# Optimization experiments

Measured on AMD Instinct MI355X. Metric: run time of the kernel, lower is better.

Reference implementation:

```python
import jax, jax.numpy as jnp
import numpy as np
from jax import lax

NBINS = 10
PP = 8            # pixels_per_cell
CPB = 2           # cells_per_block
MAX_ANGLE = float(np.pi)
EPS = 1e-5


def setup_inputs() -> dict:
    key = jax.random.key(0)
    img = jax.random.uniform(key, (32, 1, 512, 512), dtype=jnp.float32)
    # fixed Sobel-like gradient filters, same as the torch buffer: (2,1,3,3) OIHW
    m = np.array([[1.0, 0.0, -1.0], [2.0, 0.0, -2.0], [1.0, 0.0, -1.0]], dtype=np.float32)
    weight = jnp.asarray(np.stack([m, m.T])[:, None, :, :])
    return {"img": img, "weight": weight}


def reference(img, weight):
    n, _, H, W = img.shape
    # gradient conv: padding=1, stride=1 keeps spatial size
    gxy = lax.conv_general_dilated(
        img, weight, window_strides=(1, 1), padding=[(1, 1), (1, 1)],
        dimension_numbers=("NCHW", "OIHW", "NCHW"))  # (n,2,H,W)
    mag = jnp.sqrt(jnp.sum(gxy * gxy, axis=1))          # (n,H,W)
    phase = jnp.arctan2(gxy[:, 0], gxy[:, 1])           # (n,H,W)
    pbin = phase / MAX_ANGLE * NBINS
    fl = jnp.floor(pbin).astype(jnp.int32) % NBINS
    ce = jnp.ceil(pbin).astype(jnp.int32) % NBINS
    # scatter_ sets mag at floor bin (out starts at zeros), scatter_add_ adds (1-mag) at ceil bin
    oh_fl = jax.nn.one_hot(fl, NBINS, dtype=img.dtype)  # (n,H,W,nbins)
    oh_ce = jax.nn.one_hot(ce, NBINS, dtype=img.dtype)
    out = oh_fl * mag[..., None] + oh_ce * (1.0 - mag)[..., None]
    out = jnp.moveaxis(out, -1, 1)                      # (n,nbins,H,W)
    # avg pool with kernel==stride==PP, no padding -> reshape mean
    hc, wc = H // PP, W // PP
    out = out.reshape(n, NBINS, hc, PP, wc, PP).mean(axis=(3, 5))  # (n,nbins,hc,wc)
    # block normalization (L2-Hys); note: norms reduce over batch dim too, as in the source
    nbr, nbc = hc - CPB + 1, wc - CPB + 1
    blocks = jnp.stack(
        [jnp.stack([out[:, :, i:i + nbr, j:j + nbc] for j in range(CPB)], axis=2)
         for i in range(CPB)], axis=2)                  # (n,nbins,CPB,CPB,nbr,nbc)
    s = jnp.sum(blocks * blocks, axis=(0, 1, 2, 3), keepdims=True)
    v = blocks / jnp.sqrt(s + EPS * EPS)
    v = jnp.minimum(v, 0.2)
    s2 = jnp.sum(v * v, axis=(0, 1, 2, 3), keepdims=True)
    v = v / jnp.sqrt(s2 + EPS * EPS)
    return v.reshape(n, -1)  # feature_vector=True
```

## Files before the change

### kernel.cpp

```cpp
#include <hip/hip_runtime.h>
#include <math.h>

#define NBINS 10
#define NB    32
#define HH    512
#define WW    512
#define HC    64
#define WC    64
#define NBR   63
#define NBC   63
#define EPS2F 1e-10f

__global__ __launch_bounds__(256) void k_cellhist(const float* __restrict__ img,
                                                  float* __restrict__ cell,
                                                  float* __restrict__ Q) {
    const int cy = blockIdx.x;
    const int n  = blockIdx.y;
    const int t  = threadIdx.x;

    __shared__ float lds[10][516];

    const float* im = img + (size_t)n * HH * WW;
    const int gy0 = cy * 8 - 1;
    for (int idx = t; idx < 10 * 514; idx += 256) {
        int r  = idx / 514;
        int c  = idx - r * 514;
        int gr = gy0 + r, gc = c - 1;
        float v = 0.0f;
        if ((unsigned)gr < HH && (unsigned)gc < WW) v = im[gr * WW + gc];
        lds[r][c] = v;
    }
    __syncthreads();

    float hist[NBINS];
#pragma unroll
    for (int b = 0; b < NBINS; ++b) hist[b] = 0.0f;

    const float pi32 = (float)M_PI;
    const float S1 = 0.30901699f, C1 = 0.95105652f;
    const float S2 = 0.58778525f, C2 = 0.80901699f;
    const float S3 = 0.80901699f, C3 = 0.58778525f;
    const float S4 = 0.95105652f, C4 = 0.30901699f;

    const int cc   = t >> 2;
    const int sub  = t & 3;
    const int r0   = 1 + 2 * sub;
    const int stag = 2 * ((t >> 4) & 3) + sub;

    for (int ry = 0; ry < 2; ++ry) {
        const int row = r0 + ry;
        for (int k = 0; k < 8; ++k) {
            const int px  = (k + stag) & 7;
            const int col = cc * 8 + px + 1;
            float a  = lds[row - 1][col - 1];
            float b  = lds[row - 1][col    ];
            float c  = lds[row - 1][col + 1];
            float d  = lds[row    ][col - 1];
            float f  = lds[row    ][col + 1];
            float g  = lds[row + 1][col - 1];
            float h  = lds[row + 1][col    ];
            float i2 = lds[row + 1][col + 1];
            float gA = a;
            gA = gA - c;
            gA = gA + 2.0f * d;
            gA = gA - 2.0f * f;
            gA = gA + g;
            gA = gA - i2;
            float gB = a;
            gB = gB + 2.0f * b;
            gB = gB + c;
            gB = gB - g;
            gB = gB - 2.0f * h;
            gB = gB - i2;

            float mag = sqrtf(gA * gA + gB * gB);

            float y = fabsf(gA), x = fabsf(gB);
            float cr1 = fmaf(y, C1, -(x * S1));
            float cr2 = fmaf(y, C2, -(x * S2));
            float cr3 = fmaf(y, C3, -(x * S3));
            float cr4 = fmaf(y, C4, -(x * S4));
            int idx = (cr1 > 0.0f) + (cr2 > 0.0f) + (cr3 > 0.0f) + (cr4 > 0.0f);
            float minc = fminf(fminf(y, x),
                               fminf(fminf(fabsf(cr1), fabsf(cr2)),
                                     fminf(fabsf(cr3), fabsf(cr4))));
            int flm, cem;
            if (minc > 3.2e-5f * mag) {
                bool same = (gA >= 0.0f) == (gB >= 0.0f);
                flm = same ? idx : 9 - idx;
                cem = same ? idx + 1 : (idx ? 10 - idx : 0);
            } else {
                float phase = (float)atan2((double)gA, (double)gB);
                float pb = phase / pi32;
                pb = pb * 10.0f;
                int fl = (int)floorf(pb);
                int ce = (int)ceilf(pb);
                flm = fl % NBINS; if (flm < 0) flm += NBINS;
                cem = ce % NBINS; if (cem < 0) cem += NBINS;
            }
            hist[flm] += mag;
            hist[cem] += 1.0f - mag;
        }
    }

#pragma unroll
    for (int b = 0; b < NBINS; ++b) {
        hist[b] += __shfl_xor(hist[b], 1);
        hist[b] += __shfl_xor(hist[b], 2);
    }

#pragma unroll
    for (int bb = 0; bb < NBINS; ++bb) {
        if ((bb & 3) == sub)
            cell[(((size_t)n * NBINS + bb) * HC + cy) * WC + cc] = hist[bb] * 0.015625f;
    }
    if (sub == 0) {
        float q = 0.0f;
#pragma unroll
        for (int bb = 0; bb < NBINS; ++bb) {
            float cv = hist[bb] * 0.015625f;
            q = fmaf(cv, cv, q);
        }
        atomicAdd(&Q[cy * WC + cc], q);
    }
}

__global__ __launch_bounds__(256) void k_s2(const float* __restrict__ cell,
                                            const float* __restrict__ Q,
                                            float* __restrict__ s2) {
    const int i     = blockIdx.x;
    const int chunk = blockIdx.y;
    const int t     = threadIdx.x;
    const int j     = t & 63;
    const int sub   = t >> 6;
    if (j >= NBC) return;
    float s = Q[i * WC + j] + Q[i * WC + j + 1] +
              Q[(i + 1) * WC + j] + Q[(i + 1) * WC + j + 1];
    float w = 1.0f / sqrtf(s + EPS2F);
    float acc = 0.0f;
    const int nb0 = (chunk * 4 + sub) * 10;
    for (int nb = nb0; nb < nb0 + 10; ++nb) {
        const float* base = cell + ((size_t)nb * HC + i) * WC + j;
        float v00 = base[0], v01 = base[1];
        float v10 = base[WC], v11 = base[WC + 1];
        v00 = fminf(v00 * w, 0.2f); acc = fmaf(v00, v00, acc);
        v01 = fminf(v01 * w, 0.2f); acc = fmaf(v01, v01, acc);
        v10 = fminf(v10 * w, 0.2f); acc = fmaf(v10, v10, acc);
        v11 = fminf(v11 * w, 0.2f); acc = fmaf(v11, v11, acc);
    }
    atomicAdd(&s2[i * NBC + j], acc);
}

__global__ void k_inv(const float* __restrict__ Q, const float* __restrict__ s2,
                      float* __restrict__ inv1, float* __restrict__ inv2) {
    int idx = blockIdx.x * blockDim.x + threadIdx.x;
    if (idx >= NBR * NBC) return;
    int i = idx / NBC, j = idx - i * NBC;
    float s = Q[i * WC + j] + Q[i * WC + j + 1] +
              Q[(i + 1) * WC + j] + Q[(i + 1) * WC + j + 1];
    inv1[idx] = 1.0f / sqrtf(s + EPS2F);
    inv2[idx] = 1.0f / sqrtf(s2[idx] + EPS2F);
}

__global__ void k_out(const float* __restrict__ cell,
                      const float* __restrict__ inv1,
                      const float* __restrict__ inv2,
                      float* __restrict__ out) {
    int idx = blockIdx.x * blockDim.x + threadIdx.x;
    const int total = NB * NBINS * 2 * 2 * NBR * NBC;
    if (idx >= total) return;
    int ij  = idx % (NBR * NBC);
    int tmp = idx / (NBR * NBC);
    int j   = ij % NBC;
    int i   = ij / NBC;
    int dj  = tmp % 2;   tmp /= 2;
    int di  = tmp % 2;   tmp /= 2;
    int b   = tmp % NBINS;
    int n   = tmp / NBINS;
    float v = cell[(((size_t)n * NBINS + b) * HC + i + di) * WC + j + dj] * inv1[ij];
    v = fminf(v, 0.2f);
    out[idx] = v * inv2[ij];
}

extern "C" void kernel_launch(void* const* d_in, const int* in_sizes, int n_in,
                              void* d_out, int out_size, void* d_ws, size_t ws_size,
                              hipStream_t stream) {
    const float* img = (const float*)d_in[0];
    float* out = (float*)d_out;

    float* cell = (float*)d_ws;
    float* Q    = cell + (size_t)NB * NBINS * HC * WC;
    float* s2   = Q + HC * WC;
    float* inv1 = s2 + NBR * NBC;
    float* inv2 = inv1 + NBR * NBC;

    hipMemsetAsync(Q, 0, (size_t)(HC * WC + NBR * NBC) * sizeof(float), stream);
    hipLaunchKernelGGL(k_cellhist, dim3(HC, NB), dim3(256), 0, stream, img, cell, Q);
    hipLaunchKernelGGL(k_s2, dim3(NBR, 8), dim3(256), 0, stream, cell, Q, s2);
    hipLaunchKernelGGL(k_inv, dim3(16), dim3(256), 0, stream, Q, s2, inv1, inv2);
    const int total = NB * NBINS * 2 * 2 * NBR * NBC;
    hipLaunchKernelGGL(k_out, dim3((total + 255) / 256), dim3(256), 0, stream,
                       cell, inv1, inv2, out);
}
```

Before: 132.8 us.

## Accumulate cell histograms in LDS atomics and fuse normalization kernels

Per-thread register histograms indexed by dynamic bins are replaced with shared-memory atomic adds into a per-cell histogram array. This removes the dynamic register indexing, which likely spills to scratch. The s2 and inverse-norm kernels are merged into one block-per-position kernel that does a wave shuffle reduction, dropping one launch, one memset region and the global atomics. In exchange there is LDS atomic contention among the four threads sharing a cell, and the new reduction kernel has low parallelism, with 3969 blocks each reading only 320 strided elements.

```diff
diff --git a/kernel.cpp b/kernel.cpp
--- a/kernel.cpp
+++ b/kernel.cpp
@@ -19,6 +19,7 @@
     const int t  = threadIdx.x;
 
     __shared__ float lds[10][516];
+    __shared__ float chist[64][NBINS];
 
     const float* im = img + (size_t)n * HH * WW;
     const int gy0 = cy * 8 - 1;
@@ -30,11 +31,9 @@
         if ((unsigned)gr < HH && (unsigned)gc < WW) v = im[gr * WW + gc];
         lds[r][c] = v;
     }
+    for (int idx = t; idx < 64 * NBINS; idx += 256)
+        ((float*)chist)[idx] = 0.0f;
     __syncthreads();
-
-    float hist[NBINS];
-#pragma unroll
-    for (int b = 0; b < NBINS; ++b) hist[b] = 0.0f;
 
     const float pi32 = (float)M_PI;
     const float S1 = 0.30901699f, C1 = 0.95105652f;
@@ -88,7 +87,7 @@
             if (minc > 3.2e-5f * mag) {
                 bool same = (gA >= 0.0f) == (gB >= 0.0f);
                 flm = same ? idx : 9 - idx;
-                cem = same ? idx + 1 : (idx ? 10 - idx : 0);
+                cem = flm + 1; if (cem == NBINS) cem = 0;
             } else {
                 float phase = (float)atan2((double)gA, (double)gB);
                 float pb = phase / pi32;
@@ -98,68 +97,61 @@
                 flm = fl % NBINS; if (flm < 0) flm += NBINS;
                 cem = ce % NBINS; if (cem < 0) cem += NBINS;
             }
-            hist[flm] += mag;
-            hist[cem] += 1.0f - mag;
+            atomicAdd(&chist[cc][flm], mag);
+            atomicAdd(&chist[cc][cem], 1.0f - mag);
         }
     }
+    __syncthreads();
 
+    const int lane = t & 63, w = t >> 6;
 #pragma unroll
-    for (int b = 0; b < NBINS; ++b) {
-        hist[b] += __shfl_xor(hist[b], 1);
-        hist[b] += __shfl_xor(hist[b], 2);
-    }
+    for (int bb = w; bb < NBINS; bb += 4)
+        cell[(((size_t)n * NBINS + bb) * HC + cy) * WC + lane] =
+            chist[lane][bb] * 0.015625f;
 
-#pragma unroll
-    for (int bb = 0; bb < NBINS; ++bb) {
-        if ((bb & 3) == sub)
-            cell[(((size_t)n * NBINS + bb) * HC + cy) * WC + cc] = hist[bb] * 0.015625f;
-    }
-    if (sub == 0) {
+    if (t < 64) {
         float q = 0.0f;
 #pragma unroll
         for (int bb = 0; bb < NBINS; ++bb) {
-            float cv = hist[bb] * 0.015625f;
+            float cv = chist[t][bb] * 0.015625f;
             q = fmaf(cv, cv, q);
         }
-        atomicAdd(&Q[cy * WC + cc], q);
+        atomicAdd(&Q[cy * WC + t], q);
     }
 }
 
-__global__ __launch_bounds__(256) void k_s2(const float* __restrict__ cell,
-                                            const float* __restrict__ Q,
-                                            float* __restrict__ s2) {
-    const int i     = blockIdx.x;
-    const int chunk = blockIdx.y;
-    const int t     = threadIdx.x;
-    const int j     = t & 63;
-    const int sub   = t >> 6;
-    if (j >= NBC) return;
+__global__ __launch_bounds__(256) void k_norm(const float* __restrict__ cell,
+                                              const float* __restrict__ Q,
+                                              float* __restrict__ inv1,
+                                              float* __restrict__ inv2) {
+    const int ij = blockIdx.x;
+    const int i  = ij / NBC, j = ij - i * NBC;
+    const int t  = threadIdx.x;
+
     float s = Q[i * WC + j] + Q[i * WC + j + 1] +
               Q[(i + 1) * WC + j] + Q[(i + 1) * WC + j + 1];
     float w = 1.0f / sqrtf(s + EPS2F);
+
     float acc = 0.0f;
-    const int nb0 = (chunk * 4 + sub) * 10;
-    for (int nb = nb0; nb < nb0 + 10; ++nb) {
-        const float* base = cell + ((size_t)nb * HC + i) * WC + j;
-        float v00 = base[0], v01 = base[1];
+    for (int s0 = t; s0 < NB * NBINS; s0 += 256) {
+        const float* base = cell + ((size_t)s0 * HC + i) * WC + j;
+        float v00 = base[0],  v01 = base[1];
         float v10 = base[WC], v11 = base[WC + 1];
         v00 = fminf(v00 * w, 0.2f); acc = fmaf(v00, v00, acc);
         v01 = fminf(v01 * w, 0.2f); acc = fmaf(v01, v01, acc);
         v10 = fminf(v10 * w, 0.2f); acc = fmaf(v10, v10, acc);
         v11 = fminf(v11 * w, 0.2f); acc = fmaf(v11, v11, acc);
     }
-    atomicAdd(&s2[i * NBC + j], acc);
-}
-
-__global__ void k_inv(const float* __restrict__ Q, const float* __restrict__ s2,
-                      float* __restrict__ inv1, float* __restrict__ inv2) {
-    int idx = blockIdx.x * blockDim.x + threadIdx.x;
-    if (idx >= NBR * NBC) return;
-    int i = idx / NBC, j = idx - i * NBC;
-    float s = Q[i * WC + j] + Q[i * WC + j + 1] +
-              Q[(i + 1) * WC + j] + Q[(i + 1) * WC + j + 1];
-    inv1[idx] = 1.0f / sqrtf(s + EPS2F);
-    inv2[idx] = 1.0f / sqrtf(s2[idx] + EPS2F);
+#pragma unroll
+    for (int o = 1; o < 64; o <<= 1) acc += __shfl_xor(acc, o);
+    __shared__ float red[4];
+    if ((t & 63) == 0) red[t >> 6] = acc;
+    __syncthreads();
+    if (t == 0) {
+        float s2 = red[0] + red[1] + red[2] + red[3];
+        inv1[ij] = w;
+        inv2[ij] = 1.0f / sqrtf(s2 + EPS2F);
+    }
 }
 
 __global__ void k_out(const float* __restrict__ cell,
@@ -190,14 +182,13 @@
 
     float* cell = (float*)d_ws;
     float* Q    = cell + (size_t)NB * NBINS * HC * WC;
-    float* s2   = Q + HC * WC;
-    float* inv1 = s2 + NBR * NBC;
+    float* inv1 = Q + HC * WC;
     float* inv2 = inv1 + NBR * NBC;
 
-    hipMemsetAsync(Q, 0, (size_t)(HC * WC + NBR * NBC) * sizeof(float), stream);
+    hipMemsetAsync(Q, 0, (size_t)(HC * WC) * sizeof(float), stream);
     hipLaunchKernelGGL(k_cellhist, dim3(HC, NB), dim3(256), 0, stream, img, cell, Q);
-    hipLaunchKernelGGL(k_s2, dim3(NBR, 8), dim3(256), 0, stream, cell, Q, s2);
-    hipLaunchKernelGGL(k_inv, dim3(16), dim3(256), 0, stream, Q, s2, inv1, inv2);
+    hipLaunchKernelGGL(k_norm, dim3(NBR * NBC), dim3(256), 0, stream,
+                       cell, Q, inv1, inv2);
     const int total = NB * NBINS * 2 * 2 * NBR * NBC;
     hipLaunchKernelGGL(k_out, dim3((total + 255) / 256), dim3(256), 0, stream,
                        cell, inv1, inv2, out);
```

Result: slower. 199.6 us (+50.3%).
